# Performance work log

Hardware: AMD Instinct MI355X
Metric: run time of the kernel (lower is better)

The kernel has to match this reference:

```python
import jax, jax.numpy as jnp
import numpy as np

B, H, S, D = 4, 16, 2048, 128

def setup_inputs() -> dict:
    key = jax.random.key(0)
    kq, kk, kv = jax.random.split(key, 3)
    q = jax.random.normal(kq, (B, H, S, D), dtype=jnp.float32)
    k = jax.random.normal(kk, (B, H, S, D), dtype=jnp.float32)
    v = jax.random.normal(kv, (B, H, S, D), dtype=jnp.float32)
    return {"q": q, "k": k, "v": v}

def reference(q, k, v):
    # NOTE: original module applies NO 1/sqrt(d) scale.
    scores = jnp.einsum("bhqd,bhkd->bhqk", q, k)          # [B,H,S,S]
    weights = jax.nn.softmax(scores, axis=-1)
    return jnp.einsum("bhqk,bhkd->bhqd", weights, v)       # [B,H,S,D]
```

## Files before the change

### kernel.cpp

```cpp
#include <hip/hip_runtime.h>
#include <hip/hip_bf16.h>
#include <math.h>
#include <stdint.h>

#define S_LEN 2048
#define D_DIM 128

typedef _Float16 f16x8 __attribute__((ext_vector_type(8)));
typedef __fp16  fp16x2 __attribute__((ext_vector_type(2)));
typedef short bf8_t __attribute__((ext_vector_type(8)));
typedef float f32x4 __attribute__((ext_vector_type(4)));
typedef float f32x16 __attribute__((ext_vector_type(16)));
typedef unsigned int uint32x2 __attribute__((ext_vector_type(2)));
typedef _Float16 f16_t;

__device__ __forceinline__ short f2bf(float f) {
    union { float f; unsigned u; } x; x.f = f;
    unsigned u = x.u;
    u += 0x7FFF + ((u >> 16) & 1);
    return (short)(u >> 16);
}
__device__ __forceinline__ float bf2f(short h) {
    union { unsigned u; float f; } x;
    x.u = ((unsigned)(unsigned short)h) << 16;
    return x.f;
}
__device__ __forceinline__ uint32_t pkf16(float a, float b) {
    union { fp16x2 h; uint32_t u; } x;
    x.h = __builtin_amdgcn_cvt_pkrtz(a, b);
    return x.u;
}
__device__ __forceinline__ uint32x2 plswap(uint32_t a, uint32_t b) {
    return __builtin_amdgcn_permlane32_swap(a, b, false, false);
}

#define TILE_B 16384
#define WS_VT  33554432u
#define WS_NEED 67108864u

typedef const uint32_t __attribute__((address_space(1))) ga_u32;
typedef uint32_t __attribute__((address_space(3))) la_u32;
__device__ __forceinline__ void gload16(void* l, const void* g) {
    __builtin_amdgcn_global_load_lds((ga_u32*)g, (la_u32*)l, 16, 0, 0);
}

__global__ __launch_bounds__(256, 4)
void conv_kv(const float* __restrict__ K, const float* __restrict__ V,
             char* __restrict__ kf, char* __restrict__ vt)
{
    size_t tile = blockIdx.x;
    const float4* kg = (const float4*)(K + tile * (64 * 128));
    char* kd = kf + tile * TILE_B;
    #pragma unroll
    for (int it = 0; it < 8; ++it) {
        int idx = it * 256 + threadIdx.x;
        int row = idx >> 5;
        int d0  = (idx & 31) * 4;
        float4 kk = kg[idx];
        uint32_t a = pkf16(kk.x, kk.y);
        uint32_t b = pkf16(kk.z, kk.w);
        uint32_t byte = (uint32_t)((row * 256 + d0 * 2) ^ ((row & 7) << 4));
        *(uint32_t*)(kd + byte)     = a;
        *(uint32_t*)(kd + byte + 4) = b;
    }
    const float* vs = V + tile * (64 * 128);
    char* vd = vt + tile * TILE_B;
    #pragma unroll
    for (int it = 0; it < 8; ++it) {
        int idx = it * 256 + threadIdx.x;
        int d  = idx & 127;
        int k0 = (idx >> 7) * 4;
        uint32_t a = pkf16(vs[(k0 + 0) * 128 + d], vs[(k0 + 1) * 128 + d]);
        uint32_t b = pkf16(vs[(k0 + 2) * 128 + d], vs[(k0 + 3) * 128 + d]);
        uint32_t byte = (uint32_t)((d * 128 + k0 * 2) ^ ((d & 7) << 4));
        *(uint32_t*)(vd + byte)     = a;
        *(uint32_t*)(vd + byte + 4) = b;
    }
}

__global__ __launch_bounds__(256, 2)
void attn32(const float* __restrict__ Q, const char* __restrict__ ws,
            float* __restrict__ O)
{
    __shared__ __align__(16) char lds[65536];

    const int tid  = threadIdx.x;
    const int w    = tid >> 6;
    const int lane = tid & 63;
    const int ql   = lane & 31;
    const int h    = lane >> 5;

    const int fid  = blockIdx.x;
    const int nid  = (fid & 7) * 128 + (fid >> 3);
    const int qblk = nid & 15;
    const int bh   = nid >> 4;

    const size_t base = (size_t)bh * S_LEN * D_DIM;
    const int qrow0 = qblk * 128 + w * 32;

    const float L2E = 1.44269504f;
    f16x8 qf[8];
    {
        const float* qp = Q + base + (size_t)(qrow0 + ql) * D_DIM;
        #pragma unroll
        for (int c = 0; c < 8; ++c) {
            const int d0 = c * 16 + h * 8;
            float4 f0 = *(const float4*)(qp + d0);
            float4 f1 = *(const float4*)(qp + d0 + 4);
            qf[c][0] = (f16_t)(f0.x * L2E); qf[c][1] = (f16_t)(f0.y * L2E);
            qf[c][2] = (f16_t)(f0.z * L2E); qf[c][3] = (f16_t)(f0.w * L2E);
            qf[c][4] = (f16_t)(f1.x * L2E); qf[c][5] = (f16_t)(f1.y * L2E);
            qf[c][6] = (f16_t)(f1.z * L2E); qf[c][7] = (f16_t)(f1.w * L2E);
        }
    }

    f32x16 oacc[4];
    #pragma unroll
    for (int nt = 0; nt < 4; ++nt)
        #pragma unroll
        for (int r = 0; r < 16; ++r) oacc[nt][r] = 0.f;
    float m_run = -INFINITY, l_run = 0.f;

    const char* kf_t = ws + (size_t)(bh * 32) * TILE_B;
    const char* vt_t = ws + WS_VT + (size_t)(bh * 32) * TILE_B;
    const int sw = (ql & 7) << 4;

    #pragma unroll
    for (int j = 0; j < 4; ++j) {
        const int off = j * 4096 + w * 1024;
        gload16(lds + off,         kf_t + off + lane * 16);
        gload16(lds + 16384 + off, vt_t + off + lane * 16);
    }
    __syncthreads();

    int bo = 0;
    for (int t6 = 0; t6 < 32; ++t6) {
        if (t6 < 31) {
            const char* kn = kf_t + (size_t)(t6 + 1) * TILE_B;
            const char* vn = vt_t + (size_t)(t6 + 1) * TILE_B;
            const int ob = bo ^ 32768;
            #pragma unroll
            for (int j = 0; j < 4; ++j) {
                const int off = j * 4096 + w * 1024;
                gload16(lds + ob + off,         kn + off + lane * 16);
                gload16(lds + ob + 16384 + off, vn + off + lane * 16);
            }
        }

        f32x16 s0, s1;
        #pragma unroll
        for (int r = 0; r < 16; ++r) { s0[r] = 0.f; s1[r] = 0.f; }
        __builtin_amdgcn_s_setprio(1);
        #pragma unroll
        for (int c = 0; c < 8; ++c) {
            const int b0 = (ql * 256 + c * 32 + h * 16) ^ sw;
            f16x8 a0 = *(const f16x8*)(lds + bo + b0);
            f16x8 a1 = *(const f16x8*)(lds + bo + b0 + 8192);
            s0 = __builtin_amdgcn_mfma_f32_32x32x16_f16(a0, qf[c], s0, 0, 0, 0);
            s1 = __builtin_amdgcn_mfma_f32_32x32x16_f16(a1, qf[c], s1, 0, 0, 0);
        }
        __builtin_amdgcn_s_setprio(0);

        float tm = fmaxf(s0[0], s1[0]);
        #pragma unroll
        for (int r = 1; r < 16; ++r)
            tm = fmaxf(tm, fmaxf(s0[r], s1[r]));
        {
            uint32x2 ts = plswap(__float_as_uint(tm), __float_as_uint(tm));
            tm = fmaxf(__uint_as_float(ts[0]), __uint_as_float(ts[1]));
        }
        if (__any(tm > m_run + 11.f)) {
            const float mn = fmaxf(m_run, tm);
            const float sc = exp2f(m_run - mn);
            m_run = mn;
            l_run *= sc;
            #pragma unroll
            for (int r = 0; r < 16; ++r) {
                const float scq = __shfl(sc, (r & 3) + 8 * (r >> 2) + 4 * h);
                oacc[0][r] *= scq; oacc[1][r] *= scq;
                oacc[2][r] *= scq; oacc[3][r] *= scq;
            }
        }
        float ps = 0.f;
        #pragma unroll
        for (int r = 0; r < 16; ++r) {
            float p0 = exp2f(s0[r] - m_run); s0[r] = p0; ps += p0;
            float p1 = exp2f(s1[r] - m_run); s1[r] = p1; ps += p1;
        }
        {
            uint32x2 pss = plswap(__float_as_uint(ps), __float_as_uint(ps));
            ps = __uint_as_float(pss[0]) + __uint_as_float(pss[1]);
        }
        l_run += ps;

        f16x8 pf[4];
        {
            uint32_t pk[8];
            #pragma unroll
            for (int i = 0; i < 8; ++i) pk[i] = pkf16(s0[2 * i], s0[2 * i + 1]);
            uint32x2 r02 = plswap(pk[0], pk[2]), r13 = plswap(pk[1], pk[3]);
            uint32x2 r46 = plswap(pk[4], pk[6]), r57 = plswap(pk[5], pk[7]);
            union { uint32_t u[4]; f16x8 v; } b0, b1;
            b0.u[0] = r02[0]; b0.u[1] = r13[0]; b0.u[2] = r02[1]; b0.u[3] = r13[1];
            b1.u[0] = r46[0]; b1.u[1] = r57[0]; b1.u[2] = r46[1]; b1.u[3] = r57[1];
            pf[0] = b0.v; pf[1] = b1.v;
        }
        {
            uint32_t pk[8];
            #pragma unroll
            for (int i = 0; i < 8; ++i) pk[i] = pkf16(s1[2 * i], s1[2 * i + 1]);
            uint32x2 r02 = plswap(pk[0], pk[2]), r13 = plswap(pk[1], pk[3]);
            uint32x2 r46 = plswap(pk[4], pk[6]), r57 = plswap(pk[5], pk[7]);
            union { uint32_t u[4]; f16x8 v; } b0, b1;
            b0.u[0] = r02[0]; b0.u[1] = r13[0]; b0.u[2] = r02[1]; b0.u[3] = r13[1];
            b1.u[0] = r46[0]; b1.u[1] = r57[0]; b1.u[2] = r46[1]; b1.u[3] = r57[1];
            pf[2] = b0.v; pf[3] = b1.v;
        }

        __builtin_amdgcn_s_setprio(1);
        #pragma unroll
        for (int nt = 0; nt < 4; ++nt) {
            const int rb = (nt * 32 + ql) * 128;
            #pragma unroll
            for (int kc = 0; kc < 4; ++kc) {
                const int byte = (rb + kc * 32 + h * 16) ^ sw;
                f16x8 vb = *(const f16x8*)(lds + bo + 16384 + byte);
                oacc[nt] = __builtin_amdgcn_mfma_f32_32x32x16_f16(pf[kc], vb, oacc[nt], 0, 0, 0);
            }
        }
        __builtin_amdgcn_s_setprio(0);

        __syncthreads();
        bo ^= 32768;
    }

    const float inv = 1.f / l_run;
    #pragma unroll
    for (int r = 0; r < 16; ++r) {
        const int qr = (r & 3) + 8 * (r >> 2) + 4 * h;
        const float iv = __shfl(inv, qr);
        float* op = O + base + (size_t)(qrow0 + qr) * D_DIM + ql;
        op[0]  = oacc[0][r] * iv;
        op[32] = oacc[1][r] * iv;
        op[64] = oacc[2][r] * iv;
        op[96] = oacc[3][r] * iv;
    }
}

#define PADK 136
#define PADV 72
#define LDS_SHORTS 31232

__global__ __launch_bounds__(256, 2)
void attn_fwd_fb(const float* __restrict__ Q, const float* __restrict__ K,
                 const float* __restrict__ V, float* __restrict__ O)
{
    __shared__ short lds[LDS_SHORTS];
    short* khi = lds;
    short* klo = lds + 8704;
    short* vt  = lds + 17408;
    short* pls = lds + 26624;

    const int tid  = threadIdx.x;
    const int w    = tid >> 6;
    const int lane = tid & 63;
    const int lg   = lane & 15;
    const int gq   = lane >> 4;
    const int qblk = blockIdx.x;
    const int bh   = blockIdx.y;
    const size_t base = (size_t)bh * S_LEN * D_DIM;
    const int qrow0 = qblk * 64 + w * 16;

    bf8_t qhi[4], qlo[4];
    {
        const float* qp = Q + base + (size_t)(qrow0 + lg) * D_DIM;
        #pragma unroll
        for (int c = 0; c < 4; ++c) {
            const int d0 = c * 32 + gq * 8;
            #pragma unroll
            for (int j = 0; j < 8; ++j) {
                float f = qp[d0 + j];
                short hh = f2bf(f);
                qhi[c][j] = hh;
                qlo[c][j] = f2bf(f - bf2f(hh));
            }
        }
    }

    f32x4 oacc[8];
    #pragma unroll
    for (int n = 0; n < 8; ++n) oacc[n] = (f32x4){0.f, 0.f, 0.f, 0.f};
    float mrow[4] = {-INFINITY, -INFINITY, -INFINITY, -INFINITY};
    float lrow[4] = {0.f, 0.f, 0.f, 0.f};

    for (int kv = 0; kv < S_LEN; kv += 64) {
        __syncthreads();
        {
            const float4* kg = (const float4*)(K + base + (size_t)kv * D_DIM);
            const float4* vg = (const float4*)(V + base + (size_t)kv * D_DIM);
            #pragma unroll
            for (int it = 0; it < 8; ++it) {
                const int f4  = it * 256 + tid;
                const int row = f4 >> 5;
                const int d   = (f4 & 31) * 4;
                float4 kk = kg[f4];
                float4 vv = vg[f4];
                short h0 = f2bf(kk.x), h1 = f2bf(kk.y), h2 = f2bf(kk.z), h3 = f2bf(kk.w);
                short4 hw; hw.x = h0; hw.y = h1; hw.z = h2; hw.w = h3;
                *(short4*)(&khi[row * PADK + d]) = hw;
                short4 lw;
                lw.x = f2bf(kk.x - bf2f(h0));
                lw.y = f2bf(kk.y - bf2f(h1));
                lw.z = f2bf(kk.z - bf2f(h2));
                lw.w = f2bf(kk.w - bf2f(h3));
                *(short4*)(&klo[row * PADK + d]) = lw;
                vt[(d + 0) * PADV + row] = f2bf(vv.x);
                vt[(d + 1) * PADV + row] = f2bf(vv.y);
                vt[(d + 2) * PADV + row] = f2bf(vv.z);
                vt[(d + 3) * PADV + row] = f2bf(vv.w);
            }
        }
        __syncthreads();

        f32x4 sacc[4];
        #pragma unroll
        for (int t = 0; t < 4; ++t) sacc[t] = (f32x4){0.f, 0.f, 0.f, 0.f};
        #pragma unroll
        for (int t = 0; t < 4; ++t) {
            const int krow = t * 16 + lg;
            #pragma unroll
            for (int c = 0; c < 4; ++c) {
                bf8_t kh = *(const bf8_t*)(&khi[krow * PADK + c * 32 + gq * 8]);
                bf8_t kl = *(const bf8_t*)(&klo[krow * PADK + c * 32 + gq * 8]);
                sacc[t] = __builtin_amdgcn_mfma_f32_16x16x32_bf16(qhi[c], kh, sacc[t], 0, 0, 0);
                sacc[t] = __builtin_amdgcn_mfma_f32_16x16x32_bf16(qlo[c], kh, sacc[t], 0, 0, 0);
                sacc[t] = __builtin_amdgcn_mfma_f32_16x16x32_bf16(qhi[c], kl, sacc[t], 0, 0, 0);
            }
        }

        float scl[4];
        #pragma unroll
        for (int r = 0; r < 4; ++r) {
            float tm = fmaxf(fmaxf(sacc[0][r], sacc[1][r]),
                             fmaxf(sacc[2][r], sacc[3][r]));
            #pragma unroll
            for (int off = 8; off >= 1; off >>= 1)
                tm = fmaxf(tm, __shfl_xor(tm, off, 64));
            const float mn = fmaxf(mrow[r], tm);
            const float sc = __expf(mrow[r] - mn);
            float ps = 0.f;
            #pragma unroll
            for (int t = 0; t < 4; ++t) {
                float p = __expf(sacc[t][r] - mn);
                sacc[t][r] = p;
                ps += p;
            }
            #pragma unroll
            for (int off = 8; off >= 1; off >>= 1)
                ps += __shfl_xor(ps, off, 64);
            lrow[r] = lrow[r] * sc + ps;
            mrow[r] = mn;
            scl[r] = sc;
        }
        #pragma unroll
        for (int n = 0; n < 8; ++n) {
            oacc[n][0] *= scl[0];
            oacc[n][1] *= scl[1];
            oacc[n][2] *= scl[2];
            oacc[n][3] *= scl[3];
        }

        short* pw = pls + w * (16 * PADV);
        #pragma unroll
        for (int t = 0; t < 4; ++t)
            #pragma unroll
            for (int r = 0; r < 4; ++r)
                pw[(gq * 4 + r) * PADV + t * 16 + lg] = f2bf(sacc[t][r]);
        asm volatile("s_waitcnt lgkmcnt(0)" ::: "memory");

        #pragma unroll
        for (int kt = 0; kt < 2; ++kt) {
            bf8_t pa = *(const bf8_t*)(&pw[lg * PADV + kt * 32 + gq * 8]);
            #pragma unroll
            for (int n = 0; n < 8; ++n) {
                bf8_t vb = *(const bf8_t*)(&vt[(n * 16 + lg) * PADV + kt * 32 + gq * 8]);
                oacc[n] = __builtin_amdgcn_mfma_f32_16x16x32_bf16(pa, vb, oacc[n], 0, 0, 0);
            }
        }
    }

    float inv[4];
    #pragma unroll
    for (int r = 0; r < 4; ++r) inv[r] = 1.f / lrow[r];
    float* op = O + base + (size_t)qrow0 * D_DIM;
    #pragma unroll
    for (int n = 0; n < 8; ++n)
        #pragma unroll
        for (int r = 0; r < 4; ++r)
            op[(size_t)(gq * 4 + r) * D_DIM + n * 16 + lg] = oacc[n][r] * inv[r];
}

extern "C" void kernel_launch(void* const* d_in, const int* in_sizes, int n_in,
                              void* d_out, int out_size, void* d_ws, size_t ws_size,
                              hipStream_t stream) {
    const float* q = (const float*)d_in[0];
    const float* k = (const float*)d_in[1];
    const float* v = (const float*)d_in[2];
    float* o = (float*)d_out;
    if (ws_size >= (size_t)WS_NEED) {
        char* ws = (char*)d_ws;
        conv_kv<<<2048, 256, 0, stream>>>(k, v, ws, ws + WS_VT);
        attn32<<<1024, 256, 0, stream>>>(q, ws, o);
    } else {
        attn_fwd_fb<<<dim3(32, 64), 256, 0, stream>>>(q, k, v, o);
    }
}
```

Baseline: 246.9 us.

## Single-buffer K/V in LDS to double occupancy and use raw v_exp_f32

Drops the double-buffered 64 KB LDS K/V ring for a single 32 KB region and raises launch bounds from 2 to 4 blocks per CU. V for the current tile is now loaded at the top of each iteration, and the next K tile is loaded after a new mid-iteration barrier, so the loads overlap the softmax and PV work. The aim is to hide latency through more resident waves rather than explicit prefetch. It also replaces exp2f with inline v_exp_f32 and turns the serial max/sum chains into tree reductions to shorten dependency chains. The costs are an extra barrier per tile, less explicit overlap of global loads, and possible register spilling under the tighter occupancy-driven register budget.

After: 427.9 us. +73.3%, slower.

```diff
diff --git a/kernel.cpp b/kernel.cpp
--- a/kernel.cpp
+++ b/kernel.cpp
@@ -32,6 +32,11 @@
 }
 __device__ __forceinline__ uint32x2 plswap(uint32_t a, uint32_t b) {
     return __builtin_amdgcn_permlane32_swap(a, b, false, false);
+}
+__device__ __forceinline__ float exp2_fast(float x) {
+    float r;
+    asm("v_exp_f32 %0, %1" : "=v"(r) : "v"(x));
+    return r;
 }
 
 #define TILE_B 16384
@@ -78,11 +83,11 @@
     }
 }
 
-__global__ __launch_bounds__(256, 2)
+__global__ __launch_bounds__(256, 4)
 void attn32(const float* __restrict__ Q, const char* __restrict__ ws,
             float* __restrict__ O)
 {
-    __shared__ __align__(16) char lds[65536];
+    __shared__ __align__(16) char lds[32768];
 
     const int tid  = threadIdx.x;
     const int w    = tid >> 6;
@@ -128,24 +133,17 @@
     #pragma unroll
     for (int j = 0; j < 4; ++j) {
         const int off = j * 4096 + w * 1024;
-        gload16(lds + off,         kf_t + off + lane * 16);
-        gload16(lds + 16384 + off, vt_t + off + lane * 16);
+        gload16(lds + off, kf_t + off + lane * 16);
     }
     __syncthreads();
 
-    int bo = 0;
     for (int t6 = 0; t6 < 32; ++t6) {
-        if (t6 < 31) {
-            const char* kn = kf_t + (size_t)(t6 + 1) * TILE_B;
-            const char* vn = vt_t + (size_t)(t6 + 1) * TILE_B;
-            const int ob = bo ^ 32768;
-            #pragma unroll
-            for (int j = 0; j < 4; ++j) {
-                const int off = j * 4096 + w * 1024;
-                gload16(lds + ob + off,         kn + off + lane * 16);
-                gload16(lds + ob + 16384 + off, vn + off + lane * 16);
-            }
-        }
+        #pragma unroll
+        for (int j = 0; j < 4; ++j) {
+            const int off = j * 4096 + w * 1024;
+            gload16(lds + 16384 + off, vt_t + off + lane * 16);
+        }
+        vt_t += TILE_B;
 
         f32x16 s0, s1;
         #pragma unroll
@@ -154,24 +152,29 @@
         #pragma unroll
         for (int c = 0; c < 8; ++c) {
             const int b0 = (ql * 256 + c * 32 + h * 16) ^ sw;
-            f16x8 a0 = *(const f16x8*)(lds + bo + b0);
-            f16x8 a1 = *(const f16x8*)(lds + bo + b0 + 8192);
+            f16x8 a0 = *(const f16x8*)(lds + b0);
+            f16x8 a1 = *(const f16x8*)(lds + b0 + 8192);
             s0 = __builtin_amdgcn_mfma_f32_32x32x16_f16(a0, qf[c], s0, 0, 0, 0);
             s1 = __builtin_amdgcn_mfma_f32_32x32x16_f16(a1, qf[c], s1, 0, 0, 0);
         }
         __builtin_amdgcn_s_setprio(0);
 
-        float tm = fmaxf(s0[0], s1[0]);
-        #pragma unroll
-        for (int r = 1; r < 16; ++r)
-            tm = fmaxf(tm, fmaxf(s0[r], s1[r]));
+        float tmx[16];
+        #pragma unroll
+        for (int r = 0; r < 16; ++r) tmx[r] = fmaxf(s0[r], s1[r]);
+        #pragma unroll
+        for (int st = 8; st >= 1; st >>= 1)
+            #pragma unroll
+            for (int r = 0; r < 8; ++r)
+                if (r < st) tmx[r] = fmaxf(tmx[r], tmx[r + st]);
+        float tm = tmx[0];
         {
             uint32x2 ts = plswap(__float_as_uint(tm), __float_as_uint(tm));
             tm = fmaxf(__uint_as_float(ts[0]), __uint_as_float(ts[1]));
         }
         if (__any(tm > m_run + 11.f)) {
             const float mn = fmaxf(m_run, tm);
-            const float sc = exp2f(m_run - mn);
+            const float sc = exp2_fast(m_run - mn);
             m_run = mn;
             l_run *= sc;
             #pragma unroll
@@ -181,17 +184,35 @@
                 oacc[2][r] *= scq; oacc[3][r] *= scq;
             }
         }
-        float ps = 0.f;
+        float px[16];
         #pragma unroll
         for (int r = 0; r < 16; ++r) {
-            float p0 = exp2f(s0[r] - m_run); s0[r] = p0; ps += p0;
-            float p1 = exp2f(s1[r] - m_run); s1[r] = p1; ps += p1;
-        }
+            float p0 = exp2_fast(s0[r] - m_run); s0[r] = p0;
+            float p1 = exp2_fast(s1[r] - m_run); s1[r] = p1;
+            px[r] = p0 + p1;
+        }
+        #pragma unroll
+        for (int st = 8; st >= 1; st >>= 1)
+            #pragma unroll
+            for (int r = 0; r < 8; ++r)
+                if (r < st) px[r] += px[r + st];
+        float ps = px[0];
         {
             uint32x2 pss = plswap(__float_as_uint(ps), __float_as_uint(ps));
             ps = __uint_as_float(pss[0]) + __uint_as_float(pss[1]);
         }
         l_run += ps;
+
+        __syncthreads();
+
+        if (t6 < 31) {
+            kf_t += TILE_B;
+            #pragma unroll
+            for (int j = 0; j < 4; ++j) {
+                const int off = j * 4096 + w * 1024;
+                gload16(lds + off, kf_t + off + lane * 16);
+            }
+        }
 
         f16x8 pf[4];
         {
@@ -224,14 +245,13 @@
             #pragma unroll
             for (int kc = 0; kc < 4; ++kc) {
                 const int byte = (rb + kc * 32 + h * 16) ^ sw;
-                f16x8 vb = *(const f16x8*)(lds + bo + 16384 + byte);
+                f16x8 vb = *(const f16x8*)(lds + 16384 + byte);
                 oacc[nt] = __builtin_amdgcn_mfma_f32_32x32x16_f16(pf[kc], vb, oacc[nt], 0, 0, 0);
             }
         }
         __builtin_amdgcn_s_setprio(0);
 
         __syncthreads();
-        bo ^= 32768;
     }
 
     const float inv = 1.f / l_run;
```
